# Kernel optimization log

Measured on AMD Instinct MI355X. Metric: run time of the kernel, lower is better.

Reference implementation:

```python
import jax, jax.numpy as jnp
import numpy as np

A, EW, L2, NE, NA, NS, HID, OUT = 64, 112, 16, 200000, 50000, 1000000, 128, 144
Z = 2 * A + EW + L2            # 256, input width of gating linears
ELIN_IN = 2 * A + EW           # 240, input width of edge MLP


def _uniform(k, shape, fan_in):
    b = 1.0 / np.sqrt(fan_in)
    return jax.random.uniform(k, shape, jnp.float32, -b, b)


def setup_inputs() -> dict:
    key = jax.random.key(0)
    ks = jax.random.split(key, 16)
    return {
        "atom_fea": jax.random.normal(ks[0], (NA, A), jnp.float32),
        "edge_fea": jax.random.normal(ks[1], (NE, EW), jnp.float32),
        "sub_atom_idx": jax.random.randint(ks[2], (NS, 2), 0, NA),
        "sub_edge_idx": jax.random.randint(ks[3], (NS,), 0, NE),
        "sub_edge_ang": jax.random.normal(ks[4], (NS, L2), jnp.float32),
        "sub_index": jax.random.randint(ks[5], (NS,), 0, 2 * NE),
        "distance": jax.random.uniform(ks[6], (NE,), jnp.float32) * 6.0,
        "Wf": _uniform(ks[7], (Z, A), Z),
        "bf": _uniform(ks[8], (A,), Z),
        "Ws": _uniform(ks[9], (Z, A), Z),
        "bs": _uniform(ks[10], (A,), Z),
        "W1": _uniform(ks[11], (ELIN_IN, HID), ELIN_IN),
        "b1": _uniform(ks[12], (HID,), ELIN_IN),
        "W2": _uniform(ks[13], (HID, OUT), HID),
        "b2": _uniform(ks[14], (OUT,), HID),
    }


def reference(atom_fea, edge_fea, sub_atom_idx, sub_edge_idx, sub_edge_ang,
              sub_index, distance, Wf, bf, Ws, bs, W1, b1, W2, b2):
    num_edge = edge_fea.shape[0]
    # gather: [NS, 2A + EW + L2]
    z = jnp.concatenate([
        atom_fea[sub_atom_idx[:, 0]],
        atom_fea[sub_atom_idx[:, 1]],
        edge_fea[sub_edge_idx],
        sub_edge_ang,
    ], axis=-1)
    # gated MLP: sigmoid(lin_f) * softplus(lin_s)
    out = jax.nn.sigmoid(z @ Wf + bf) * jax.nn.softplus(z @ Ws + bs)
    # if_exp: exponential distance decay, sigma=3, n=2
    decay = jnp.exp(-(distance[sub_edge_idx] ** 2) / (3.0 ** 2) / 2.0)
    out = out * decay[:, None]
    # scatter_add into 2*num_edge slots, then split into the two edge halves
    agg = jax.ops.segment_sum(out, sub_index, num_segments=2 * num_edge)
    agg = agg.reshape(num_edge, 2, A)
    h = jnp.concatenate([agg[:, 0, :], agg[:, 1, :], edge_fea], axis=-1)
    # e_lin: Linear -> SiLU -> Linear
    return jax.nn.silu(h @ W1 + b1) @ W2 + b2
```

## Files before the change

kernel.cpp:

```cpp
#include <hip/hip_runtime.h>
#include <stdint.h>

#define NAtoms   50000
#define NEdges   200000
#define NSubs    1000000
#define KP1      776
#define GCH      32


typedef short  s16x8 __attribute__((ext_vector_type(8)));
typedef unsigned short u16x8 __attribute__((ext_vector_type(8)));
typedef float  f32x4 __attribute__((ext_vector_type(4)));

__device__ __forceinline__ float bf2f(unsigned short u) {
    union { unsigned int i; float f; } v; v.i = ((unsigned int)u) << 16; return v.f;
}
__device__ __forceinline__ unsigned short f2bf(float f) {
    union { float f; unsigned int i; } v; v.f = f;
    unsigned int x = v.i;
    unsigned int r = (x + 0x7fffu + ((x >> 16) & 1u)) >> 16;
    return (unsigned short)r;
}
__device__ __forceinline__ unsigned short f2bf_hw(float f) {
    union { __bf16 h; unsigned short u; } v; v.h = (__bf16)f; return v.u;
}
__device__ __forceinline__ s16x8 pk_bf16x8(f32x4 a, f32x4 b) {
    union { u16x8 u; s16x8 s; } o;
    o.u[0] = f2bf_hw(a[0]); o.u[1] = f2bf_hw(a[1]); o.u[2] = f2bf_hw(a[2]); o.u[3] = f2bf_hw(a[3]);
    o.u[4] = f2bf_hw(b[0]); o.u[5] = f2bf_hw(b[1]); o.u[6] = f2bf_hw(b[2]); o.u[7] = f2bf_hw(b[3]);
    return o.s;
}

typedef const __attribute__((address_space(1))) void* as1_cvp;
typedef __attribute__((address_space(3))) void* as3_vp;
__device__ __forceinline__ void gll16(const void* g, void* l) {
    __builtin_amdgcn_global_load_lds((as1_cvp)g, (as3_vp)l, 16, 0, 0);
}

__global__ void k_prep(const float* __restrict__ Wf, const float* __restrict__ Ws,
                       const float* __restrict__ W1, const float* __restrict__ W2,
                       unsigned short* __restrict__ WTfs, unsigned short* __restrict__ WT1,
                       unsigned short* __restrict__ WT2) {
    int id = blockIdx.x * 256 + threadIdx.x;
    if (id < 32768) {
        int k = id & 255, n = id >> 8;
        WTfs[n * 256 + k] = f2bf((n < 64) ? Wf[k * 64 + n] : Ws[k * 64 + (n - 64)]);
    } else if (id < 131072) {
        int m = id - 32768;
        int n = m / 768, k = m - n * 768;
        int seg = k >> 8, kk = k & 255;
        float w = (kk < 240) ? W1[kk * 128 + n] : 0.0f;
        unsigned short hi = f2bf(w);
        WT1[n * 768 + k] = (seg < 2) ? hi : f2bf(w - bf2f(hi));
    } else if (id < 149504) {
        int m = id - 131072;
        int k = m & 127, n = m >> 7;
        WT2[n * 128 + k] = f2bf(W2[k * 144 + n]);
    }
}

__global__ __launch_bounds__(256) void k_gate(
    const float* __restrict__ atom, const float* __restrict__ edge,
    const int* __restrict__ sai, const int* __restrict__ sei,
    const float* __restrict__ ang, const int* __restrict__ sidx_g,
    const float* __restrict__ dist,
    const float* __restrict__ bfv, const float* __restrict__ bsv,
    const unsigned short* __restrict__ WTfs, float* __restrict__ aggf) {
    __shared__ __align__(16) float ztf[GCH * 256];
    __shared__ float decf[GCH];
    __shared__ int   sidx[GCH];

    const int t = threadIdx.x;
    const int w = t >> 6;
    const int l = t & 63;
    const int l15 = l & 15, q = l >> 4;
    const int rowBlock = blockIdx.x << 8;

    s16x8 bF[8], bS[8];
    {
        const unsigned short* pf = WTfs + (w * 16 + l15) * 256 + q * 8;
        const unsigned short* ps = WTfs + (64 + w * 16 + l15) * 256 + q * 8;
#pragma unroll
        for (int kb = 0; kb < 8; ++kb) {
            bF[kb] = *(const s16x8*)(pf + kb * 32);
            bS[kb] = *(const s16x8*)(ps + kb * 32);
        }
    }
    const float bfj = bfv[w * 16 + l15];
    const float bsj = bsv[w * 16 + l15];

    for (int c = 0; c < 8; ++c) {
        const int chunkBase = rowBlock + c * GCH;

        int sA[8], i0A[8], i1A[8], e2A[8];
#pragma unroll
        for (int p = 0; p < 8; ++p) {
            int s = chunkBase + w * 8 + p;
            s = (s < NSubs) ? s : (NSubs - 1);
            s = __builtin_amdgcn_readfirstlane(s);
            sA[p] = s;
            i0A[p] = sai[2 * s];
            i1A[p] = sai[2 * s + 1];
            e2A[p] = sei[s];
        }
#pragma unroll
        for (int p = 0; p < 8; ++p) {
            const int lr = w * 8 + p;
            const int G = l ^ (lr & 7);
            const float* srcA = atom + (size_t)i0A[p] * 64  + (G      ) * 4;
            const float* srcB = atom + (size_t)i1A[p] * 64  + (G - 16 ) * 4;
            const float* srcC = edge + (size_t)e2A[p] * 112 + (G - 32 ) * 4;
            const float* srcD = ang  + (size_t)sA[p]  * 16  + (G - 60 ) * 4;
            const float* src = (G < 16) ? srcA : (G < 32) ? srcB : (G < 60) ? srcC : srcD;
            gll16(src, &ztf[lr * 256]);
            float d = dist[e2A[p]];
            float dc = __expf(-d * d * (1.0f / 18.0f));
            int sv = sidx_g[sA[p]];
            if (l == 0) { decf[lr] = dc; sidx[lr] = sv; }
        }
        asm volatile("s_waitcnt vmcnt(0)" ::: "memory");
        __syncthreads();

#pragma unroll
        for (int mb = 0; mb < 2; ++mb) {
            f32x4 aF = {0.f, 0.f, 0.f, 0.f}, aS = {0.f, 0.f, 0.f, 0.f};
            const int row = mb * 16 + l15;
            const int sw = row & 7;
            const float* zrow = ztf + row * 256;
#pragma unroll
            for (int kb = 0; kb < 8; ++kb) {
                const int g0 = kb * 8 + q * 2;
                f32x4 x0 = *(const f32x4*)(zrow + (((g0    ) ^ sw) << 2));
                f32x4 x1 = *(const f32x4*)(zrow + (((g0 + 1) ^ sw) << 2));
                s16x8 a = pk_bf16x8(x0, x1);
                aF = __builtin_amdgcn_mfma_f32_16x16x32_bf16(a, bF[kb], aF, 0, 0, 0);
                aS = __builtin_amdgcn_mfma_f32_16x16x32_bf16(a, bS[kb], aS, 0, 0, 0);
            }
#pragma unroll
            for (int r = 0; r < 4; ++r) {
                int lr = mb * 16 + q * 4 + r;
                int s = chunkBase + lr;
                if (s < NSubs) {
                    float xf = aF[r] + bfj;
                    float xs = aS[r] + bsj;
                    float sig = __builtin_amdgcn_rcpf(1.0f + __expf(-xf));
                    float sp  = (xs > 20.0f) ? xs : __logf(1.0f + __expf(xs));
                    float val = sig * sp * decf[lr];
                    unsafeAtomicAdd(aggf + (size_t)sidx[lr] * 64 + (w * 16 + l15), val);
                }
            }
        }
        __syncthreads();
    }
}

__global__ __launch_bounds__(256) void k_elin1(
    const float* __restrict__ aggf, const float* __restrict__ edge,
    const unsigned short* __restrict__ WT1, const float* __restrict__ b1,
    unsigned short* __restrict__ hid) {
    __shared__ __align__(16) unsigned short zt[32 * KP1];

    const int t = threadIdx.x;
    const int w = t >> 6;
    const int l = t & 63;
    const int l15 = l & 15, q = l >> 4;
    const int rowBlock = blockIdx.x << 7;

    const float b1a = b1[w * 16 + l15];
    const float b1b = b1[64 + w * 16 + l15];

    const int cg = t & 31;
    const int g  = t >> 5;

    for (int c = 0; c < 4; ++c) {
        const int chunkBase = rowBlock + c * 32;
        f32x4 v0a[4], v1a[4];
#pragma unroll
        for (int i = 0; i < 4; ++i) {
            int lr = i * 8 + g;
            int e = chunkBase + lr;
            int ec = (e < NEdges) ? e : (NEdges - 1);
            f32x4 v0 = {0.f, 0.f, 0.f, 0.f}, v1 = {0.f, 0.f, 0.f, 0.f};
            if (cg < 16) {
                const float* src = aggf + (size_t)ec * 128 + cg * 8;
                v0 = *(const f32x4*)src; v1 = *(const f32x4*)(src + 4);
            } else if (cg < 30) {
                const float* src = edge + (size_t)ec * 112 + (cg - 16) * 8;
                v0 = *(const f32x4*)src; v1 = *(const f32x4*)(src + 4);
            }
            v0a[i] = v0; v1a[i] = v1;
        }
#pragma unroll
        for (int i = 0; i < 4; ++i) {
            int lr = i * 8 + g;
            u16x8 hi, lo;
#pragma unroll
            for (int j = 0; j < 4; ++j) {
                hi[j] = f2bf_hw(v0a[i][j]);     lo[j] = f2bf_hw(v0a[i][j] - bf2f(hi[j]));
                hi[4 + j] = f2bf_hw(v1a[i][j]); lo[4 + j] = f2bf_hw(v1a[i][j] - bf2f(hi[4 + j]));
            }
            unsigned short* zrow = zt + lr * KP1;
            *(u16x8*)(zrow + cg * 8) = hi;
            *(u16x8*)(zrow + 256 + cg * 8) = lo;
            *(u16x8*)(zrow + 512 + cg * 8) = hi;
        }
        __syncthreads();
#pragma unroll
        for (int mb = 0; mb < 2; ++mb) {
            f32x4 aA = {0.f, 0.f, 0.f, 0.f}, aB = {0.f, 0.f, 0.f, 0.f};
            const unsigned short* zb = zt + (mb * 16 + l15) * KP1 + q * 8;
            const unsigned short* pa = WT1 + (w * 16 + l15) * 768 + q * 8;
            const unsigned short* pb = WT1 + (64 + w * 16 + l15) * 768 + q * 8;
#pragma unroll
            for (int kb = 0; kb < 24; ++kb) {
                s16x8 a  = *(const s16x8*)(zb + kb * 32);
                s16x8 ba = *(const s16x8*)(pa + kb * 32);
                s16x8 bb = *(const s16x8*)(pb + kb * 32);
                aA = __builtin_amdgcn_mfma_f32_16x16x32_bf16(a, ba, aA, 0, 0, 0);
                aB = __builtin_amdgcn_mfma_f32_16x16x32_bf16(a, bb, aB, 0, 0, 0);
            }
#pragma unroll
            for (int r = 0; r < 4; ++r) {
                int e = chunkBase + mb * 16 + q * 4 + r;
                if (e < NEdges) {
                    float xa = aA[r] + b1a;
                    float xb = aB[r] + b1b;
                    float sa = xa * __builtin_amdgcn_rcpf(1.0f + __expf(-xa));
                    float sb = xb * __builtin_amdgcn_rcpf(1.0f + __expf(-xb));
                    hid[e * 128 + w * 16 + l15]      = f2bf_hw(sa);
                    hid[e * 128 + 64 + w * 16 + l15] = f2bf_hw(sb);
                }
            }
        }
        __syncthreads();
    }
}

__global__ __launch_bounds__(256) void k_elin2(
    const unsigned short* __restrict__ hid, const unsigned short* __restrict__ WT2,
    const float* __restrict__ b2, float* __restrict__ out) {
    const int t = threadIdx.x;
    const int w = t >> 6;
    const int l = t & 63;
    const int l15 = l & 15, q = l >> 4;
    const int rb = blockIdx.x * 64 + w * 16;

    f32x4 acc[9];
#pragma unroll
    for (int nb = 0; nb < 9; ++nb) acc[nb] = (f32x4){0.f, 0.f, 0.f, 0.f};

#pragma unroll
    for (int kb = 0; kb < 4; ++kb) {
        s16x8 a = *(const s16x8*)(hid + (rb + l15) * 128 + kb * 32 + q * 8);
#pragma unroll
        for (int nb = 0; nb < 9; ++nb) {
            s16x8 b = *(const s16x8*)(WT2 + (nb * 16 + l15) * 128 + kb * 32 + q * 8);
            acc[nb] = __builtin_amdgcn_mfma_f32_16x16x32_bf16(a, b, acc[nb], 0, 0, 0);
        }
    }
#pragma unroll
    for (int nb = 0; nb < 9; ++nb) {
        int n = nb * 16 + l15;
        float bb = b2[n];
#pragma unroll
        for (int r = 0; r < 4; ++r) {
            int e = rb + q * 4 + r;
            out[e * 144 + n] = acc[nb][r] + bb;
        }
    }
}

extern "C" void kernel_launch(void* const* d_in, const int* in_sizes, int n_in,
                              void* d_out, int out_size, void* d_ws, size_t ws_size,
                              hipStream_t stream) {
    const float* atom = (const float*)d_in[0];
    const float* edge = (const float*)d_in[1];
    const int*   sai  = (const int*)d_in[2];
    const int*   sei  = (const int*)d_in[3];
    const float* ang  = (const float*)d_in[4];
    const int*   sidx = (const int*)d_in[5];
    const float* dist = (const float*)d_in[6];
    const float* Wf   = (const float*)d_in[7];
    const float* bfv  = (const float*)d_in[8];
    const float* Ws   = (const float*)d_in[9];
    const float* bsv  = (const float*)d_in[10];
    const float* W1   = (const float*)d_in[11];
    const float* b1   = (const float*)d_in[12];
    const float* W2   = (const float*)d_in[13];
    const float* b2   = (const float*)d_in[14];
    float* out = (float*)d_out;

    const size_t AGG_BYTES = (size_t)2 * NEdges * 64 * sizeof(float);
    const size_t HID_OFF   = AGG_BYTES;
    const size_t WTFS_OFF  = HID_OFF + (size_t)NEdges * 128 * 2;
    const size_t WT1_OFF   = WTFS_OFF + 128 * 256 * 2;
    const size_t WT2_OFF   = WT1_OFF + 128 * 768 * 2;
    const size_t NEEDED    = WT2_OFF + 144 * 128 * 2;
    if (ws_size < NEEDED) return;

    char* ws = (char*)d_ws;
    float* aggf = (float*)ws;
    unsigned short* hid  = (unsigned short*)(ws + HID_OFF);
    unsigned short* WTfs = (unsigned short*)(ws + WTFS_OFF);
    unsigned short* WT1  = (unsigned short*)(ws + WT1_OFF);
    unsigned short* WT2  = (unsigned short*)(ws + WT2_OFF);

    hipMemsetAsync(aggf, 0, AGG_BYTES, stream);
    k_prep<<<584, 256, 0, stream>>>(Wf, Ws, W1, W2, WTfs, WT1, WT2);
    k_gate<<<(NSubs + 255) / 256, 256, 0, stream>>>(atom, edge, sai, sei, ang, sidx, dist,
                                                    bfv, bsv, WTfs, aggf);
    k_elin1<<<(NEdges + 127) / 128, 256, 0, stream>>>(aggf, edge, WT1, b1, hid);
    k_elin2<<<NEdges / 64, 256, 0, stream>>>(hid, WT2, b2, out);
}
```

Before: 822.9 us.

## Double-buffer gather staging in gating kernel to overlap loads with MFMA

The gating kernel now keeps two LDS staging buffers, plus per-chunk decay and index slots. It issues the global-to-LDS gather for the next chunk of 32 subs before computing the current one, replacing the per-chunk full vmcnt(0) drain with a partial vmcnt(8) wait and raw s_barriers. Index loads for chunk c+2 are prefetched into the freed register set. The goal is to hide gather latency behind the MFMA, activation and atomic work. In exchange, the LDS footprint doubles, which lowers how many blocks can be resident per CU, and correctness depends on the hand-tuned waitcnt counts.

Measured after the change: 805.9 us. -2.1%, faster.

```diff
diff --git a/kernel.cpp b/kernel.cpp
--- a/kernel.cpp
+++ b/kernel.cpp
@@ -66,9 +66,9 @@
     const float* __restrict__ dist,
     const float* __restrict__ bfv, const float* __restrict__ bsv,
     const unsigned short* __restrict__ WTfs, float* __restrict__ aggf) {
-    __shared__ __align__(16) float ztf[GCH * 256];
-    __shared__ float decf[GCH];
-    __shared__ int   sidx[GCH];
+    __shared__ __align__(16) float ztf[2][GCH * 256];
+    __shared__ float decf[2][GCH];
+    __shared__ int   sidx[2][GCH];
 
     const int t = threadIdx.x;
     const int w = t >> 6;
@@ -89,44 +89,45 @@
     const float bfj = bfv[w * 16 + l15];
     const float bsj = bsv[w * 16 + l15];
 
-    for (int c = 0; c < 8; ++c) {
-        const int chunkBase = rowBlock + c * GCH;
-
-        int sA[8], i0A[8], i1A[8], e2A[8];
+    int sA[2][8], i0A[2][8], i1A[2][8], e2A[2][8];
+
+    auto LOADIDX = [&](int cc, int par) {
 #pragma unroll
         for (int p = 0; p < 8; ++p) {
-            int s = chunkBase + w * 8 + p;
+            int s = rowBlock + cc * GCH + w * 8 + p;
             s = (s < NSubs) ? s : (NSubs - 1);
             s = __builtin_amdgcn_readfirstlane(s);
-            sA[p] = s;
-            i0A[p] = sai[2 * s];
-            i1A[p] = sai[2 * s + 1];
-            e2A[p] = sei[s];
-        }
+            sA[par][p] = s;
+            i0A[par][p] = sai[2 * s];
+            i1A[par][p] = sai[2 * s + 1];
+            e2A[par][p] = sei[s];
+        }
+    };
+    auto ISSUE = [&](int par) {
 #pragma unroll
         for (int p = 0; p < 8; ++p) {
             const int lr = w * 8 + p;
             const int G = l ^ (lr & 7);
-            const float* srcA = atom + (size_t)i0A[p] * 64  + (G      ) * 4;
-            const float* srcB = atom + (size_t)i1A[p] * 64  + (G - 16 ) * 4;
-            const float* srcC = edge + (size_t)e2A[p] * 112 + (G - 32 ) * 4;
-            const float* srcD = ang  + (size_t)sA[p]  * 16  + (G - 60 ) * 4;
+            const float* srcA = atom + (size_t)i0A[par][p] * 64  + (G      ) * 4;
+            const float* srcB = atom + (size_t)i1A[par][p] * 64  + (G - 16 ) * 4;
+            const float* srcC = edge + (size_t)e2A[par][p] * 112 + (G - 32 ) * 4;
+            const float* srcD = ang  + (size_t)sA[par][p]  * 16  + (G - 60 ) * 4;
             const float* src = (G < 16) ? srcA : (G < 32) ? srcB : (G < 60) ? srcC : srcD;
-            gll16(src, &ztf[lr * 256]);
-            float d = dist[e2A[p]];
+            gll16(src, &ztf[par][lr * 256]);
+            float d = dist[e2A[par][p]];
             float dc = __expf(-d * d * (1.0f / 18.0f));
-            int sv = sidx_g[sA[p]];
-            if (l == 0) { decf[lr] = dc; sidx[lr] = sv; }
-        }
-        asm volatile("s_waitcnt vmcnt(0)" ::: "memory");
-        __syncthreads();
-
+            int sv = sidx_g[sA[par][p]];
+            if (l == 0) { decf[par][lr] = dc; sidx[par][lr] = sv; }
+        }
+    };
+    auto COMPUTE = [&](int cc, int par) {
+        const int chunkBase = rowBlock + cc * GCH;
 #pragma unroll
         for (int mb = 0; mb < 2; ++mb) {
             f32x4 aF = {0.f, 0.f, 0.f, 0.f}, aS = {0.f, 0.f, 0.f, 0.f};
             const int row = mb * 16 + l15;
             const int sw = row & 7;
-            const float* zrow = ztf + row * 256;
+            const float* zrow = &ztf[par][row * 256];
 #pragma unroll
             for (int kb = 0; kb < 8; ++kb) {
                 const int g0 = kb * 8 + q * 2;
@@ -145,13 +146,38 @@
                     float xs = aS[r] + bsj;
                     float sig = __builtin_amdgcn_rcpf(1.0f + __expf(-xf));
                     float sp  = (xs > 20.0f) ? xs : __logf(1.0f + __expf(xs));
-                    float val = sig * sp * decf[lr];
-                    unsafeAtomicAdd(aggf + (size_t)sidx[lr] * 64 + (w * 16 + l15), val);
+                    float val = sig * sp * decf[par][lr];
+                    unsafeAtomicAdd(aggf + (size_t)sidx[par][lr] * 64 + (w * 16 + l15), val);
                 }
             }
         }
-        __syncthreads();
-    }
+    };
+
+    LOADIDX(0, 0);
+    ISSUE(0);
+    LOADIDX(1, 1);
+
+#pragma unroll
+    for (int c = 0; c < 7; ++c) {
+        const int pc = c & 1;
+        const int pn = (c + 1) & 1;
+        ISSUE(pn);
+        if (c + 2 < 8) LOADIDX(c + 2, pc);
+        asm volatile("s_waitcnt vmcnt(8)" ::: "memory");
+        asm volatile("s_waitcnt lgkmcnt(0)" ::: "memory");
+        __builtin_amdgcn_sched_barrier(0);
+        __builtin_amdgcn_s_barrier();
+        __builtin_amdgcn_sched_barrier(0);
+        COMPUTE(c, pc);
+        asm volatile("s_waitcnt lgkmcnt(0)" ::: "memory");
+        __builtin_amdgcn_s_barrier();
+        __builtin_amdgcn_sched_barrier(0);
+    }
+    asm volatile("s_waitcnt vmcnt(0) lgkmcnt(0)" ::: "memory");
+    __builtin_amdgcn_sched_barrier(0);
+    __builtin_amdgcn_s_barrier();
+    __builtin_amdgcn_sched_barrier(0);
+    COMPUTE(7, 1);
 }
 
 __global__ __launch_bounds__(256) void k_elin1(
```
